# Kernel optimization log

Hardware: AMD Instinct MI355X
Metric: run time of the kernel (lower is better)

The kernel has to match this reference:

```python
import jax, jax.numpy as jnp
import numpy as np

BN_EPS = 1e-5


def conv2d(x, w, b, s, p):
    out = jax.lax.conv_general_dilated(
        x, w, (s, s), [(p, p), (p, p)],
        dimension_numbers=('NCHW', 'OIHW', 'NCHW'))
    return out + b[None, :, None, None]


def deform_conv2d(x, offset, mask, weight, s, p):
    # x: [B,C,H,W]; offset: [B,2*k*k,Ho,Wo] (y,x interleaved per tap);
    # mask: [B,k*k,Ho,Wo]; weight: [O,C,k,k]
    B, C, H, W = x.shape
    O, _, k, _ = weight.shape
    T = k * k
    Ho, Wo = offset.shape[2], offset.shape[3]
    off = offset.reshape(B, T, 2, Ho, Wo)
    ii = jnp.repeat(jnp.arange(k), k).astype(x.dtype)  # kernel row per tap
    jj = jnp.tile(jnp.arange(k), k).astype(x.dtype)    # kernel col per tap
    base_y = (jnp.arange(Ho) * s - p).astype(x.dtype)
    base_x = (jnp.arange(Wo) * s - p).astype(x.dtype)
    py = base_y[None, None, :, None] + ii[None, :, None, None] + off[:, :, 0]  # [B,T,Ho,Wo]
    px = base_x[None, None, None, :] + jj[None, :, None, None] + off[:, :, 1]
    y0 = jnp.floor(py)
    x0 = jnp.floor(px)
    ly = py - y0
    lx = px - x0
    y0i = y0.astype(jnp.int32)
    x0i = x0.astype(jnp.int32)
    x_flat = x.reshape(B, C, H * W)

    def gather(yy, xx):
        valid = ((yy >= 0) & (yy < H) & (xx >= 0) & (xx < W)).astype(x.dtype)
        idx = jnp.clip(yy, 0, H - 1) * W + jnp.clip(xx, 0, W - 1)
        idx_f = jnp.broadcast_to(idx.reshape(B, 1, -1), (B, C, T * Ho * Wo))
        g = jnp.take_along_axis(x_flat, idx_f, axis=2).reshape(B, C, T, Ho, Wo)
        return g * valid[:, None]

    val = (((1 - ly) * (1 - lx))[:, None] * gather(y0i, x0i)
           + ((1 - ly) * lx)[:, None] * gather(y0i, x0i + 1)
           + (ly * (1 - lx))[:, None] * gather(y0i + 1, x0i)
           + (ly * lx)[:, None] * gather(y0i + 1, x0i + 1))
    val = val * mask[:, None]  # modulated samples [B,C,T,Ho,Wo]
    w_flat = weight.reshape(O, C, T)
    return jnp.einsum('bcthw,oct->bohw', val, w_flat)


def setup_inputs() -> dict:
    key = jax.random.key(0)
    ks = jax.random.split(key, 8)
    B, C1, C2, H, W, k = 4, 128, 128, 64, 64, 3
    fan_in = C1 * k * k
    return {
        'x': jax.random.normal(ks[0], (B, C1, H, W), jnp.float32),
        'offset_w': 0.01 * jax.random.normal(ks[1], (2 * k * k, C1, k, k), jnp.float32),
        'offset_b': jnp.zeros((2 * k * k,), jnp.float32),
        'mask_w': 0.01 * jax.random.normal(ks[2], (k * k, C1, k, k), jnp.float32),
        'mask_b': jnp.zeros((k * k,), jnp.float32),
        'weight': jax.random.normal(ks[3], (C2, C1, k, k), jnp.float32) / np.sqrt(fan_in),
        'bn_gamma': 0.5 + jax.random.uniform(ks[4], (C2,), jnp.float32),
        'bn_beta': 0.1 * jax.random.normal(ks[5], (C2,), jnp.float32),
        'bn_mean': 0.1 * jax.random.normal(ks[6], (C2,), jnp.float32),
        'bn_var': 0.5 + jax.random.uniform(ks[7], (C2,), jnp.float32),
    }


def reference(x, offset_w, offset_b, mask_w, mask_b, weight,
              bn_gamma, bn_beta, bn_mean, bn_var):
    s, p = 1, 1
    offset = conv2d(x, offset_w, offset_b, s, p)
    mask = jax.nn.sigmoid(conv2d(x, mask_w, mask_b, s, p))
    out = deform_conv2d(x, offset, mask, weight, s, p)
    scale = bn_gamma / jnp.sqrt(bn_var + BN_EPS)
    out = (out - bn_mean[None, :, None, None]) * scale[None, :, None, None] \
        + bn_beta[None, :, None, None]
    return out * jax.nn.sigmoid(out)  # SiLU
```

## Files before the change

### kernel.cpp

```cpp
#include <hip/hip_runtime.h>
#include <math.h>

typedef unsigned short u16;
typedef short bf16x8 __attribute__((ext_vector_type(8)));
typedef float f32x4 __attribute__((ext_vector_type(4)));

#define XT_B   0u
#define WF_B   4194304u
#define WRF_B  4489216u
#define BNS_B  4562944u
#define BNB_B  4563456u

__device__ __forceinline__ u16 f2bf(float f) {
  union { float f; unsigned int i; } v; v.f = f;
  unsigned int i = v.i;
  return (u16)((i + 0x7fffu + ((i >> 16) & 1u)) >> 16);
}
__device__ __forceinline__ float ulo(unsigned int u) {
  union { unsigned int i; float f; } v; v.i = u << 16; return v.f;
}
__device__ __forceinline__ float uhi(unsigned int u) {
  union { unsigned int i; float f; } v; v.i = u & 0xffff0000u; return v.f;
}
__device__ __forceinline__ unsigned int pk(float lo, float hi) {
  return (unsigned int)f2bf(lo) | ((unsigned int)f2bf(hi) << 16);
}

__global__ __launch_bounds__(256) void prep_kernel(
    const float* __restrict__ x,   const float* __restrict__ ow,
    const float* __restrict__ mw,  const float* __restrict__ wgt,
    const float* __restrict__ gam, const float* __restrict__ bet,
    const float* __restrict__ mean,const float* __restrict__ var,
    char* __restrict__ wsb) {
  int blk = blockIdx.x, tid = threadIdx.x;
  if (blk < 512) {
    __shared__ u16 tile[32][136];
    int b = blk >> 7, y = (blk >> 1) & 63, xh = blk & 1;
    const float* src = x + (size_t)b * 524288 + y * 64 + xh * 32;
#pragma unroll
    for (int r = 0; r < 4; ++r) {
      int flat = r * 256 + tid;
      int c = flat >> 3, x4 = (flat & 7) * 4;
      float4 v = *(const float4*)(src + c * 4096 + x4);
      tile[x4 + 0][c] = f2bf(v.x);
      tile[x4 + 1][c] = f2bf(v.y);
      tile[x4 + 2][c] = f2bf(v.z);
      tile[x4 + 3][c] = f2bf(v.w);
    }
    __syncthreads();
    u16* dst = (u16*)(wsb + XT_B) + ((b * 64 + y) * 64 + xh * 32) * 128;
#pragma unroll
    for (int r = 0; r < 2; ++r) {
      int flat = r * 256 + tid;
      int xx = flat >> 4, c8 = (flat & 15) * 8;
      *(uint4*)(dst + xx * 128 + c8) = *(const uint4*)&tile[xx][c8];
    }
  } else if (blk < 1088) {
    int idx = (blk - 512) * 256 + tid;
    int jj = idx & 7, l = (idx >> 3) & 63, ks = (idx >> 9) & 3,
        mt = (idx >> 11) & 7, t = idx >> 14;
    int o = mt * 16 + (l & 15);
    int c = ks * 32 + (l >> 4) * 8 + jj;
    ((u16*)(wsb + WF_B))[idx] = f2bf(wgt[(o * 128 + c) * 9 + t]);
  } else if (blk < 1232) {
    int idx = (blk - 1088) * 256 + tid;
    int jj = idx & 7, l = (idx >> 3) & 63, mt = (idx >> 9) & 1, ks = idx >> 10;
    int oc = mt * 16 + (l & 15);
    int k = ks * 32 + (l >> 4) * 8 + jj;
    int t = k >> 7, c = k & 127;
    float v = 0.f;
    if (oc < 18) v = ow[(oc * 128 + c) * 9 + t];
    else if (oc < 27) v = mw[((oc - 18) * 128 + c) * 9 + t];
    ((u16*)(wsb + WRF_B))[idx] = f2bf(v);
  } else {
    if (tid < 128) {
      float s = gam[tid] * rsqrtf(var[tid] + 1e-5f);
      ((float*)(wsb + BNS_B))[tid] = s;
      ((float*)(wsb + BNB_B))[tid] = bet[tid] - mean[tid] * s;
    }
  }
}

__global__ __launch_bounds__(256, 4) void main_kernel(
    const char* __restrict__ wsb, const float* __restrict__ ob,
    const float* __restrict__ mb, float* __restrict__ out) {
  __shared__ __align__(16) char smem[16 * 1160 * 2];
  __shared__ float soff[16][32];
  u16* vbuf = (u16*)smem;
  float* pred = (float*)smem;

  int blk = blockIdx.x;
  int b = blk >> 8, ho = (blk >> 2) & 63, qd = blk & 3;
  int p0 = qd * 16;
  int tid = threadIdx.x;
  int w = tid >> 6, l = tid & 63, quad = l >> 4, pn = l & 15;

  const u16* XT = (const u16*)(wsb + XT_B);
  const bf16x8* WFv = (const bf16x8*)(wsb + WF_B);
  const bf16x8* WRFv = (const bf16x8*)(wsb + WRF_B);
  bf16x8 bz = {0, 0, 0, 0, 0, 0, 0, 0};

  {
    int mt = w & 1, kh = w >> 1;
    f32x4 acc = {0.f, 0.f, 0.f, 0.f};
#pragma unroll
    for (int t = 0; t < 9; ++t) {
      int y = ho + t / 3 - 1;
      int xx = p0 + pn + t % 3 - 1;
      bool valid = ((unsigned)y < 64u) && ((unsigned)xx < 64u);
      const u16* bp = XT + ((b * 64 + y) * 64 + xx) * 128 + quad * 8;
#pragma unroll
      for (int kqi = 0; kqi < 2; ++kqi) {
        int kq = kh * 2 + kqi;
        bf16x8 a = WRFv[((t * 4 + kq) * 2 + mt) * 64 + l];
        bf16x8 bb = valid ? *(const bf16x8*)(bp + kq * 32) : bz;
        acc = __builtin_amdgcn_mfma_f32_16x16x32_bf16(a, bb, acc, 0, 0, 0);
      }
    }
#pragma unroll
    for (int r = 0; r < 4; ++r)
      pred[((kh * 2 + mt) * 16 + quad * 4 + r) * 16 + pn] = acc[r];
  }
  __syncthreads();
  for (int i = tid; i < 432; i += 256) {
    int oc = i >> 4, p = i & 15;
    int mt = oc >> 4, row = oc & 15;
    float v = pred[(mt * 16 + row) * 16 + p] + pred[((2 + mt) * 16 + row) * 16 + p]
            + (oc < 18 ? ob[oc] : mb[oc - 18]);
    if (oc >= 18) v = 1.f / (1.f + __expf(-v));
    soff[p][oc] = v;
  }
  __syncthreads();

  {
    int cl = l & 15, pi = l >> 4;
    int p = w * 4 + pi;
    const u16* xb = XT + (size_t)b * 524288 + cl * 8;
#pragma unroll
    for (int t = 0; t < 9; ++t) {
      float oy = soff[p][2 * t], ox = soff[p][2 * t + 1], m = soff[p][18 + t];
      float py = (float)(ho + t / 3 - 1) + oy;
      float px = (float)(p0 + p + t % 3 - 1) + ox;
      float y0f = floorf(py), x0f = floorf(px);
      int y0 = (int)y0f, x0 = (int)x0f;
      float ly = py - y0f, lx = px - x0f;
      float vy0 = (y0 >= 0 && y0 < 64) ? 1.f : 0.f;
      float vy1 = (y0 >= -1 && y0 < 63) ? 1.f : 0.f;
      float vx0 = (x0 >= 0 && x0 < 64) ? 1.f : 0.f;
      float vx1 = (x0 >= -1 && x0 < 63) ? 1.f : 0.f;
      int y0c = min(max(y0, 0), 63), y1c = min(max(y0 + 1, 0), 63);
      int x0c = min(max(x0, 0), 63), x1c = min(max(x0 + 1, 0), 63);
      uint4 q00 = *(const uint4*)(xb + (y0c * 64 + x0c) * 128);
      uint4 q01 = *(const uint4*)(xb + (y0c * 64 + x1c) * 128);
      uint4 q10 = *(const uint4*)(xb + (y1c * 64 + x0c) * 128);
      uint4 q11 = *(const uint4*)(xb + (y1c * 64 + x1c) * 128);
      float w00 = (1.f - ly) * (1.f - lx) * m * vy0 * vx0;
      float w01 = (1.f - ly) * lx * m * vy0 * vx1;
      float w10 = ly * (1.f - lx) * m * vy1 * vx0;
      float w11 = ly * lx * m * vy1 * vx1;
      uint4 o;
      o.x = pk(w00 * ulo(q00.x) + w01 * ulo(q01.x) + w10 * ulo(q10.x) + w11 * ulo(q11.x),
               w00 * uhi(q00.x) + w01 * uhi(q01.x) + w10 * uhi(q10.x) + w11 * uhi(q11.x));
      o.y = pk(w00 * ulo(q00.y) + w01 * ulo(q01.y) + w10 * ulo(q10.y) + w11 * ulo(q11.y),
               w00 * uhi(q00.y) + w01 * uhi(q01.y) + w10 * uhi(q10.y) + w11 * uhi(q11.y));
      o.z = pk(w00 * ulo(q00.z) + w01 * ulo(q01.z) + w10 * ulo(q10.z) + w11 * ulo(q11.z),
               w00 * uhi(q00.z) + w01 * uhi(q01.z) + w10 * uhi(q10.z) + w11 * uhi(q11.z));
      o.w = pk(w00 * ulo(q00.w) + w01 * ulo(q01.w) + w10 * ulo(q10.w) + w11 * ulo(q11.w),
               w00 * uhi(q00.w) + w01 * uhi(q01.w) + w10 * uhi(q10.w) + w11 * uhi(q11.w));
      *(uint4*)&vbuf[p * 1160 + t * 128 + cl * 8] = o;
    }
  }
  __syncthreads();

  f32x4 acc0 = {0.f, 0.f, 0.f, 0.f}, acc1 = {0.f, 0.f, 0.f, 0.f};
  bf16x8 A0[2][4], A1[2][4];
#pragma unroll
  for (int ks = 0; ks < 4; ++ks) {
    A0[0][ks] = WFv[((0 * 8 + 2 * w) * 4 + ks) * 64 + l];
    A1[0][ks] = WFv[((0 * 8 + 2 * w + 1) * 4 + ks) * 64 + l];
  }
#pragma unroll
  for (int t = 0; t < 9; ++t) {
    int cur = t & 1, nxt = cur ^ 1;
    if (t < 8) {
#pragma unroll
      for (int ks = 0; ks < 4; ++ks) {
        A0[nxt][ks] = WFv[(((t + 1) * 8 + 2 * w) * 4 + ks) * 64 + l];
        A1[nxt][ks] = WFv[(((t + 1) * 8 + 2 * w + 1) * 4 + ks) * 64 + l];
      }
    }
#pragma unroll
    for (int ks = 0; ks < 4; ++ks) {
      bf16x8 bfr = *(const bf16x8*)&vbuf[pn * 1160 + t * 128 + ks * 32 + quad * 8];
      acc0 = __builtin_amdgcn_mfma_f32_16x16x32_bf16(A0[cur][ks], bfr, acc0, 0, 0, 0);
      acc1 = __builtin_amdgcn_mfma_f32_16x16x32_bf16(A1[cur][ks], bfr, acc1, 0, 0, 0);
    }
  }

  const float* BNS = (const float*)(wsb + BNS_B);
  const float* BNB = (const float*)(wsb + BNB_B);
#pragma unroll
  for (int mi = 0; mi < 2; ++mi) {
    f32x4 acc = mi ? acc1 : acc0;
#pragma unroll
    for (int r = 0; r < 4; ++r) {
      int o = (2 * w + mi) * 16 + quad * 4 + r;
      float v = acc[r] * BNS[o] + BNB[o];
      v = v / (1.f + __expf(-v));
      out[((b * 128 + o) * 64 + ho) * 64 + p0 + pn] = v;
    }
  }
}

extern "C" void kernel_launch(void* const* d_in, const int* in_sizes, int n_in,
                              void* d_out, int out_size, void* d_ws, size_t ws_size,
                              hipStream_t stream) {
  const float* x    = (const float*)d_in[0];
  const float* ow   = (const float*)d_in[1];
  const float* ob   = (const float*)d_in[2];
  const float* mw   = (const float*)d_in[3];
  const float* mb   = (const float*)d_in[4];
  const float* wgt  = (const float*)d_in[5];
  const float* gam  = (const float*)d_in[6];
  const float* bet  = (const float*)d_in[7];
  const float* mean = (const float*)d_in[8];
  const float* var  = (const float*)d_in[9];
  char* wsb = (char*)d_ws;
  float* out = (float*)d_out;

  prep_kernel<<<1233, 256, 0, stream>>>(x, ow, mw, wgt, gam, bet, mean, var, wsb);
  main_kernel<<<1024, 256, 0, stream>>>(wsb, ob, mb, out);
}
```

Measured before the change: 106.1 us.

## Double block tile to 32 pixels with 8 waves and software-pipeline bilinear gathers

Each block now covers 32 output pixels with 512 threads. Each wave owns one 16-channel output tile and reuses its weight fragments across two pixel tiles, which halves per-wave global weight loads. The bilinear-sampling loop is software-pipelined so the gathers for tap t+1 are issued before tap t is combined, hiding gather latency. The cost is twice the LDS per block, higher register pressure, and only 512 blocks, which lowers occupancy and grid parallelism.

```diff
diff --git a/kernel.cpp b/kernel.cpp
--- a/kernel.cpp
+++ b/kernel.cpp
@@ -81,17 +81,17 @@
   }
 }
 
-__global__ __launch_bounds__(256, 4) void main_kernel(
+__global__ __launch_bounds__(512, 4) void main_kernel(
     const char* __restrict__ wsb, const float* __restrict__ ob,
     const float* __restrict__ mb, float* __restrict__ out) {
-  __shared__ __align__(16) char smem[16 * 1160 * 2];
-  __shared__ float soff[16][32];
+  __shared__ __align__(16) char smem[32 * 1160 * 2];
+  __shared__ float soff[32][32];
   u16* vbuf = (u16*)smem;
   float* pred = (float*)smem;
 
   int blk = blockIdx.x;
-  int b = blk >> 8, ho = (blk >> 2) & 63, qd = blk & 3;
-  int p0 = qd * 16;
+  int b = blk >> 7, ho = (blk >> 1) & 63, half = blk & 1;
+  int p0 = half * 32;
   int tid = threadIdx.x;
   int w = tid >> 6, l = tid & 63, quad = l >> 4, pn = l & 15;
 
@@ -101,12 +101,13 @@
   bf16x8 bz = {0, 0, 0, 0, 0, 0, 0, 0};
 
   {
-    int mt = w & 1, kh = w >> 1;
+    int mt = w & 1, nt = (w >> 1) & 1, kh = w >> 2;
+    int p = nt * 16 + pn;
     f32x4 acc = {0.f, 0.f, 0.f, 0.f};
 #pragma unroll
     for (int t = 0; t < 9; ++t) {
       int y = ho + t / 3 - 1;
-      int xx = p0 + pn + t % 3 - 1;
+      int xx = p0 + p + t % 3 - 1;
       bool valid = ((unsigned)y < 64u) && ((unsigned)xx < 64u);
       const u16* bp = XT + ((b * 64 + y) * 64 + xx) * 128 + quad * 8;
 #pragma unroll
@@ -119,13 +120,14 @@
     }
 #pragma unroll
     for (int r = 0; r < 4; ++r)
-      pred[((kh * 2 + mt) * 16 + quad * 4 + r) * 16 + pn] = acc[r];
+      pred[(((kh * 2 + mt) * 2 + nt) * 16 + quad * 4 + r) * 16 + pn] = acc[r];
   }
   __syncthreads();
-  for (int i = tid; i < 432; i += 256) {
-    int oc = i >> 4, p = i & 15;
-    int mt = oc >> 4, row = oc & 15;
-    float v = pred[(mt * 16 + row) * 16 + p] + pred[((2 + mt) * 16 + row) * 16 + p]
+  for (int i = tid; i < 864; i += 512) {
+    int oc = i >> 5, p = i & 31;
+    int mt = oc >> 4, row = oc & 15, nt = p >> 4, pn2 = p & 15;
+    float v = pred[((mt * 2 + nt) * 16 + row) * 16 + pn2]
+            + pred[(((2 + mt) * 2 + nt) * 16 + row) * 16 + pn2]
             + (oc < 18 ? ob[oc] : mb[oc - 18]);
     if (oc >= 18) v = 1.f / (1.f + __expf(-v));
     soff[p][oc] = v;
@@ -136,8 +138,10 @@
     int cl = l & 15, pi = l >> 4;
     int p = w * 4 + pi;
     const u16* xb = XT + (size_t)b * 524288 + cl * 8;
-#pragma unroll
-    for (int t = 0; t < 9; ++t) {
+    uint4 q00[2], q01[2], q10[2], q11[2];
+    float w00[2], w01[2], w10[2], w11[2];
+
+    auto issue = [&](int t, int st) {
       float oy = soff[p][2 * t], ox = soff[p][2 * t + 1], m = soff[p][18 + t];
       float py = (float)(ho + t / 3 - 1) + oy;
       float px = (float)(p0 + p + t % 3 - 1) + ox;
@@ -150,64 +154,70 @@
       float vx1 = (x0 >= -1 && x0 < 63) ? 1.f : 0.f;
       int y0c = min(max(y0, 0), 63), y1c = min(max(y0 + 1, 0), 63);
       int x0c = min(max(x0, 0), 63), x1c = min(max(x0 + 1, 0), 63);
-      uint4 q00 = *(const uint4*)(xb + (y0c * 64 + x0c) * 128);
-      uint4 q01 = *(const uint4*)(xb + (y0c * 64 + x1c) * 128);
-      uint4 q10 = *(const uint4*)(xb + (y1c * 64 + x0c) * 128);
-      uint4 q11 = *(const uint4*)(xb + (y1c * 64 + x1c) * 128);
-      float w00 = (1.f - ly) * (1.f - lx) * m * vy0 * vx0;
-      float w01 = (1.f - ly) * lx * m * vy0 * vx1;
-      float w10 = ly * (1.f - lx) * m * vy1 * vx0;
-      float w11 = ly * lx * m * vy1 * vx1;
+      q00[st] = *(const uint4*)(xb + (y0c * 64 + x0c) * 128);
+      q01[st] = *(const uint4*)(xb + (y0c * 64 + x1c) * 128);
+      q10[st] = *(const uint4*)(xb + (y1c * 64 + x0c) * 128);
+      q11[st] = *(const uint4*)(xb + (y1c * 64 + x1c) * 128);
+      w00[st] = (1.f - ly) * (1.f - lx) * m * vy0 * vx0;
+      w01[st] = (1.f - ly) * lx * m * vy0 * vx1;
+      w10[st] = ly * (1.f - lx) * m * vy1 * vx0;
+      w11[st] = ly * lx * m * vy1 * vx1;
+    };
+
+    issue(0, 0);
+#pragma unroll
+    for (int t = 0; t < 9; ++t) {
+      int cur = t & 1;
+      if (t < 8) issue(t + 1, cur ^ 1);
+      float a00 = w00[cur], a01 = w01[cur], a10 = w10[cur], a11 = w11[cur];
+      uint4 c00 = q00[cur], c01 = q01[cur], c10 = q10[cur], c11 = q11[cur];
       uint4 o;
-      o.x = pk(w00 * ulo(q00.x) + w01 * ulo(q01.x) + w10 * ulo(q10.x) + w11 * ulo(q11.x),
-               w00 * uhi(q00.x) + w01 * uhi(q01.x) + w10 * uhi(q10.x) + w11 * uhi(q11.x));
-      o.y = pk(w00 * ulo(q00.y) + w01 * ulo(q01.y) + w10 * ulo(q10.y) + w11 * ulo(q11.y),
-               w00 * uhi(q00.y) + w01 * uhi(q01.y) + w10 * uhi(q10.y) + w11 * uhi(q11.y));
-      o.z = pk(w00 * ulo(q00.z) + w01 * ulo(q01.z) + w10 * ulo(q10.z) + w11 * ulo(q11.z),
-               w00 * uhi(q00.z) + w01 * uhi(q01.z) + w10 * uhi(q10.z) + w11 * uhi(q11.z));
-      o.w = pk(w00 * ulo(q00.w) + w01 * ulo(q01.w) + w10 * ulo(q10.w) + w11 * ulo(q11.w),
-               w00 * uhi(q00.w) + w01 * uhi(q01.w) + w10 * uhi(q10.w) + w11 * uhi(q11.w));
+      o.x = pk(a00 * ulo(c00.x) + a01 * ulo(c01.x) + a10 * ulo(c10.x) + a11 * ulo(c11.x),
+               a00 * uhi(c00.x) + a01 * uhi(c01.x) + a10 * uhi(c10.x) + a11 * uhi(c11.x));
+      o.y = pk(a00 * ulo(c00.y) + a01 * ulo(c01.y) + a10 * ulo(c10.y) + a11 * ulo(c11.y),
+               a00 * uhi(c00.y) + a01 * uhi(c01.y) + a10 * uhi(c10.y) + a11 * uhi(c11.y));
+      o.z = pk(a00 * ulo(c00.z) + a01 * ulo(c01.z) + a10 * ulo(c10.z) + a11 * ulo(c11.z),
+               a00 * uhi(c00.z) + a01 * uhi(c01.z) + a10 * uhi(c10.z) + a11 * uhi(c11.z));
+      o.w = pk(a00 * ulo(c00.w) + a01 * ulo(c01.w) + a10 * ulo(c10.w) + a11 * ulo(c11.w),
+               a00 * uhi(c00.w) + a01 * uhi(c01.w) + a10 * uhi(c10.w) + a11 * uhi(c11.w));
       *(uint4*)&vbuf[p * 1160 + t * 128 + cl * 8] = o;
     }
   }
   __syncthreads();
 
   f32x4 acc0 = {0.f, 0.f, 0.f, 0.f}, acc1 = {0.f, 0.f, 0.f, 0.f};
-  bf16x8 A0[2][4], A1[2][4];
-#pragma unroll
-  for (int ks = 0; ks < 4; ++ks) {
-    A0[0][ks] = WFv[((0 * 8 + 2 * w) * 4 + ks) * 64 + l];
-    A1[0][ks] = WFv[((0 * 8 + 2 * w + 1) * 4 + ks) * 64 + l];
-  }
+  bf16x8 A[2][4];
+#pragma unroll
+  for (int ks = 0; ks < 4; ++ks)
+    A[0][ks] = WFv[((0 * 8 + w) * 4 + ks) * 64 + l];
 #pragma unroll
   for (int t = 0; t < 9; ++t) {
     int cur = t & 1, nxt = cur ^ 1;
     if (t < 8) {
 #pragma unroll
-      for (int ks = 0; ks < 4; ++ks) {
-        A0[nxt][ks] = WFv[(((t + 1) * 8 + 2 * w) * 4 + ks) * 64 + l];
-        A1[nxt][ks] = WFv[(((t + 1) * 8 + 2 * w + 1) * 4 + ks) * 64 + l];
-      }
+      for (int ks = 0; ks < 4; ++ks)
+        A[nxt][ks] = WFv[(((t + 1) * 8 + w) * 4 + ks) * 64 + l];
     }
 #pragma unroll
     for (int ks = 0; ks < 4; ++ks) {
-      bf16x8 bfr = *(const bf16x8*)&vbuf[pn * 1160 + t * 128 + ks * 32 + quad * 8];
-      acc0 = __builtin_amdgcn_mfma_f32_16x16x32_bf16(A0[cur][ks], bfr, acc0, 0, 0, 0);
-      acc1 = __builtin_amdgcn_mfma_f32_16x16x32_bf16(A1[cur][ks], bfr, acc1, 0, 0, 0);
+      bf16x8 b0 = *(const bf16x8*)&vbuf[pn * 1160 + t * 128 + ks * 32 + quad * 8];
+      bf16x8 b1 = *(const bf16x8*)&vbuf[(16 + pn) * 1160 + t * 128 + ks * 32 + quad * 8];
+      acc0 = __builtin_amdgcn_mfma_f32_16x16x32_bf16(A[cur][ks], b0, acc0, 0, 0, 0);
+      acc1 = __builtin_amdgcn_mfma_f32_16x16x32_bf16(A[cur][ks], b1, acc1, 0, 0, 0);
     }
   }
 
   const float* BNS = (const float*)(wsb + BNS_B);
   const float* BNB = (const float*)(wsb + BNB_B);
 #pragma unroll
-  for (int mi = 0; mi < 2; ++mi) {
-    f32x4 acc = mi ? acc1 : acc0;
+  for (int nt = 0; nt < 2; ++nt) {
+    f32x4 acc = nt ? acc1 : acc0;
 #pragma unroll
     for (int r = 0; r < 4; ++r) {
-      int o = (2 * w + mi) * 16 + quad * 4 + r;
+      int o = w * 16 + quad * 4 + r;
       float v = acc[r] * BNS[o] + BNB[o];
       v = v / (1.f + __expf(-v));
-      out[((b * 128 + o) * 64 + ho) * 64 + p0 + pn] = v;
+      out[((b * 128 + o) * 64 + ho) * 64 + p0 + nt * 16 + pn] = v;
     }
   }
 }
@@ -229,5 +239,5 @@
   float* out = (float*)d_out;
 
   prep_kernel<<<1233, 256, 0, stream>>>(x, ow, mw, wgt, gam, bet, mean, var, wsb);
-  main_kernel<<<1024, 256, 0, stream>>>(wsb, ob, mb, out);
-}
+  main_kernel<<<512, 512, 0, stream>>>(wsb, ob, mb, out);
+}
```

Measured after the change: 105.6 us. No clear change (-0.5%).

## Feed bilinear samples directly into MFMA with split-K across waves

Applied to the files above, without the earlier changes.

The main kernel no longer stages the modulated bilinear samples in a shared-memory buffer. Each wave now owns a 32-channel slice of K and feeds the freshly computed bf16 fragment straight into MFMAs for all 8 output tiles, holding 8 accumulators per wave. The partial sums from the four waves are reduced through a padded shared array before BN and SiLU. This removes the LDS write/read round trip and one barrier, at the cost of more accumulator registers (and possible occupancy loss) plus a cross-wave reduction. Weight fragments are now loaded inline per tap instead of being double-buffered.

```diff
diff --git a/kernel.cpp b/kernel.cpp
--- a/kernel.cpp
+++ b/kernel.cpp
@@ -84,10 +84,9 @@
 __global__ __launch_bounds__(256, 4) void main_kernel(
     const char* __restrict__ wsb, const float* __restrict__ ob,
     const float* __restrict__ mb, float* __restrict__ out) {
-  __shared__ __align__(16) char smem[16 * 1160 * 2];
-  __shared__ float soff[16][32];
-  u16* vbuf = (u16*)smem;
-  float* pred = (float*)smem;
+  __shared__ __align__(16) float red[4][8][16][17];
+  __shared__ float sofft[28 * 17];
+  float* pred = &red[0][0][0][0];
 
   int blk = blockIdx.x;
   int b = blk >> 8, ho = (blk >> 2) & 63, qd = blk & 3;
@@ -128,19 +127,22 @@
     float v = pred[(mt * 16 + row) * 16 + p] + pred[((2 + mt) * 16 + row) * 16 + p]
             + (oc < 18 ? ob[oc] : mb[oc - 18]);
     if (oc >= 18) v = 1.f / (1.f + __expf(-v));
-    soff[p][oc] = v;
+    sofft[oc * 17 + p] = v;
   }
   __syncthreads();
 
+  f32x4 acc[8];
+#pragma unroll
+  for (int ot = 0; ot < 8; ++ot) acc[ot] = (f32x4){0.f, 0.f, 0.f, 0.f};
   {
-    int cl = l & 15, pi = l >> 4;
-    int p = w * 4 + pi;
-    const u16* xb = XT + (size_t)b * 524288 + cl * 8;
+    const u16* xb = XT + (size_t)b * 524288 + w * 32 + quad * 8;
 #pragma unroll
     for (int t = 0; t < 9; ++t) {
-      float oy = soff[p][2 * t], ox = soff[p][2 * t + 1], m = soff[p][18 + t];
+      float oy = sofft[(2 * t) * 17 + pn];
+      float ox = sofft[(2 * t + 1) * 17 + pn];
+      float m  = sofft[(18 + t) * 17 + pn];
       float py = (float)(ho + t / 3 - 1) + oy;
-      float px = (float)(p0 + p + t % 3 - 1) + ox;
+      float px = (float)(p0 + pn + t % 3 - 1) + ox;
       float y0f = floorf(py), x0f = floorf(px);
       int y0 = (int)y0f, x0 = (int)x0f;
       float ly = py - y0f, lx = px - x0f;
@@ -158,57 +160,42 @@
       float w01 = (1.f - ly) * lx * m * vy0 * vx1;
       float w10 = ly * (1.f - lx) * m * vy1 * vx0;
       float w11 = ly * lx * m * vy1 * vx1;
-      uint4 o;
-      o.x = pk(w00 * ulo(q00.x) + w01 * ulo(q01.x) + w10 * ulo(q10.x) + w11 * ulo(q11.x),
-               w00 * uhi(q00.x) + w01 * uhi(q01.x) + w10 * uhi(q10.x) + w11 * uhi(q11.x));
-      o.y = pk(w00 * ulo(q00.y) + w01 * ulo(q01.y) + w10 * ulo(q10.y) + w11 * ulo(q11.y),
-               w00 * uhi(q00.y) + w01 * uhi(q01.y) + w10 * uhi(q10.y) + w11 * uhi(q11.y));
-      o.z = pk(w00 * ulo(q00.z) + w01 * ulo(q01.z) + w10 * ulo(q10.z) + w11 * ulo(q11.z),
-               w00 * uhi(q00.z) + w01 * uhi(q01.z) + w10 * uhi(q10.z) + w11 * uhi(q11.z));
-      o.w = pk(w00 * ulo(q00.w) + w01 * ulo(q01.w) + w10 * ulo(q10.w) + w11 * ulo(q11.w),
-               w00 * uhi(q00.w) + w01 * uhi(q01.w) + w10 * uhi(q10.w) + w11 * uhi(q11.w));
-      *(uint4*)&vbuf[p * 1160 + t * 128 + cl * 8] = o;
-    }
-  }
+      union { uint4 u; bf16x8 v; } bq;
+      bq.u.x = pk(w00 * ulo(q00.x) + w01 * ulo(q01.x) + w10 * ulo(q10.x) + w11 * ulo(q11.x),
+                  w00 * uhi(q00.x) + w01 * uhi(q01.x) + w10 * uhi(q10.x) + w11 * uhi(q11.x));
+      bq.u.y = pk(w00 * ulo(q00.y) + w01 * ulo(q01.y) + w10 * ulo(q10.y) + w11 * ulo(q11.y),
+                  w00 * uhi(q00.y) + w01 * uhi(q01.y) + w10 * uhi(q10.y) + w11 * uhi(q11.y));
+      bq.u.z = pk(w00 * ulo(q00.z) + w01 * ulo(q01.z) + w10 * ulo(q10.z) + w11 * ulo(q11.z),
+                  w00 * uhi(q00.z) + w01 * uhi(q01.z) + w10 * uhi(q10.z) + w11 * uhi(q11.z));
+      bq.u.w = pk(w00 * ulo(q00.w) + w01 * ulo(q01.w) + w10 * ulo(q10.w) + w11 * ulo(q11.w),
+                  w00 * uhi(q00.w) + w01 * uhi(q01.w) + w10 * uhi(q10.w) + w11 * uhi(q11.w));
+#pragma unroll
+      for (int ot = 0; ot < 8; ++ot) {
+        bf16x8 a = WFv[((t * 8 + ot) * 4 + w) * 64 + l];
+        acc[ot] = __builtin_amdgcn_mfma_f32_16x16x32_bf16(a, bq.v, acc[ot], 0, 0, 0);
+      }
+    }
+  }
+
+#pragma unroll
+  for (int ot = 0; ot < 8; ++ot)
+#pragma unroll
+    for (int r = 0; r < 4; ++r)
+      red[w][ot][quad * 4 + r][pn] = acc[ot][r];
   __syncthreads();
-
-  f32x4 acc0 = {0.f, 0.f, 0.f, 0.f}, acc1 = {0.f, 0.f, 0.f, 0.f};
-  bf16x8 A0[2][4], A1[2][4];
-#pragma unroll
-  for (int ks = 0; ks < 4; ++ks) {
-    A0[0][ks] = WFv[((0 * 8 + 2 * w) * 4 + ks) * 64 + l];
-    A1[0][ks] = WFv[((0 * 8 + 2 * w + 1) * 4 + ks) * 64 + l];
-  }
-#pragma unroll
-  for (int t = 0; t < 9; ++t) {
-    int cur = t & 1, nxt = cur ^ 1;
-    if (t < 8) {
-#pragma unroll
-      for (int ks = 0; ks < 4; ++ks) {
-        A0[nxt][ks] = WFv[(((t + 1) * 8 + 2 * w) * 4 + ks) * 64 + l];
-        A1[nxt][ks] = WFv[(((t + 1) * 8 + 2 * w + 1) * 4 + ks) * 64 + l];
-      }
-    }
-#pragma unroll
-    for (int ks = 0; ks < 4; ++ks) {
-      bf16x8 bfr = *(const bf16x8*)&vbuf[pn * 1160 + t * 128 + ks * 32 + quad * 8];
-      acc0 = __builtin_amdgcn_mfma_f32_16x16x32_bf16(A0[cur][ks], bfr, acc0, 0, 0, 0);
-      acc1 = __builtin_amdgcn_mfma_f32_16x16x32_bf16(A1[cur][ks], bfr, acc1, 0, 0, 0);
-    }
-  }
 
   const float* BNS = (const float*)(wsb + BNS_B);
   const float* BNB = (const float*)(wsb + BNB_B);
 #pragma unroll
-  for (int mi = 0; mi < 2; ++mi) {
-    f32x4 acc = mi ? acc1 : acc0;
-#pragma unroll
-    for (int r = 0; r < 4; ++r) {
-      int o = (2 * w + mi) * 16 + quad * 4 + r;
-      float v = acc[r] * BNS[o] + BNB[o];
-      v = v / (1.f + __expf(-v));
-      out[((b * 128 + o) * 64 + ho) * 64 + p0 + pn] = v;
-    }
+  for (int i = 0; i < 8; ++i) {
+    int idx = i * 256 + tid;
+    int o = idx >> 4, p = idx & 15;
+    int ot = o >> 4, row = o & 15;
+    float s = red[0][ot][row][p] + red[1][ot][row][p]
+            + red[2][ot][row][p] + red[3][ot][row][p];
+    float v = s * BNS[o] + BNB[o];
+    v = v / (1.f + __expf(-v));
+    out[((b * 128 + o) * 64 + ho) * 64 + p0 + p] = v;
   }
 }
 
```

New measurement: 116.2 us. +9.5%, slower.

## Double threads per block and split offset conv, sampling and GEMM across 8 waves

Applied to the files above, without the earlier changes.

Raises the main kernel from 256 to 512 threads (8 waves) with the same 16-pixel tile. The offset/mask conv now splits K four ways across waves and reduces 4 partials. The bilinear sampling splits the 9 taps between two wave halves, and the output GEMM gives each wave one 16-channel tile instead of two. The offset buffer is transposed with padding to avoid bank conflicts. The aim is more waves in flight to hide gather latency and fewer registers per thread. The costs are more block-level sync overhead, a higher occupancy target in the launch bounds that may force register limits, and less ILP per wave.

```diff
diff --git a/kernel.cpp b/kernel.cpp
--- a/kernel.cpp
+++ b/kernel.cpp
@@ -81,13 +81,12 @@
   }
 }
 
-__global__ __launch_bounds__(256, 4) void main_kernel(
+__global__ __launch_bounds__(512, 8) void main_kernel(
     const char* __restrict__ wsb, const float* __restrict__ ob,
     const float* __restrict__ mb, float* __restrict__ out) {
-  __shared__ __align__(16) char smem[16 * 1160 * 2];
-  __shared__ float soff[16][32];
-  u16* vbuf = (u16*)smem;
-  float* pred = (float*)smem;
+  __shared__ __align__(16) u16 vbuf[16 * 1160];
+  __shared__ float sofft[28 * 17];
+  float* pred = (float*)vbuf;
 
   int blk = blockIdx.x;
   int b = blk >> 8, ho = (blk >> 2) & 63, qd = blk & 3;
@@ -101,7 +100,7 @@
   bf16x8 bz = {0, 0, 0, 0, 0, 0, 0, 0};
 
   {
-    int mt = w & 1, kh = w >> 1;
+    int mt = w & 1, kq = w >> 1;
     f32x4 acc = {0.f, 0.f, 0.f, 0.f};
 #pragma unroll
     for (int t = 0; t < 9; ++t) {
@@ -109,36 +108,41 @@
       int xx = p0 + pn + t % 3 - 1;
       bool valid = ((unsigned)y < 64u) && ((unsigned)xx < 64u);
       const u16* bp = XT + ((b * 64 + y) * 64 + xx) * 128 + quad * 8;
-#pragma unroll
-      for (int kqi = 0; kqi < 2; ++kqi) {
-        int kq = kh * 2 + kqi;
-        bf16x8 a = WRFv[((t * 4 + kq) * 2 + mt) * 64 + l];
-        bf16x8 bb = valid ? *(const bf16x8*)(bp + kq * 32) : bz;
-        acc = __builtin_amdgcn_mfma_f32_16x16x32_bf16(a, bb, acc, 0, 0, 0);
-      }
+      bf16x8 a = WRFv[((t * 4 + kq) * 2 + mt) * 64 + l];
+      bf16x8 bb = valid ? *(const bf16x8*)(bp + kq * 32) : bz;
+      acc = __builtin_amdgcn_mfma_f32_16x16x32_bf16(a, bb, acc, 0, 0, 0);
     }
 #pragma unroll
     for (int r = 0; r < 4; ++r)
-      pred[((kh * 2 + mt) * 16 + quad * 4 + r) * 16 + pn] = acc[r];
+      pred[(w * 16 + quad * 4 + r) * 16 + pn] = acc[r];
   }
   __syncthreads();
-  for (int i = tid; i < 432; i += 256) {
-    int oc = i >> 4, p = i & 15;
+  if (tid < 432) {
+    int oc = tid >> 4, p = tid & 15;
     int mt = oc >> 4, row = oc & 15;
-    float v = pred[(mt * 16 + row) * 16 + p] + pred[((2 + mt) * 16 + row) * 16 + p]
+    float v = pred[((0 * 2 + mt) * 16 + row) * 16 + p]
+            + pred[((1 * 2 + mt) * 16 + row) * 16 + p]
+            + pred[((2 * 2 + mt) * 16 + row) * 16 + p]
+            + pred[((3 * 2 + mt) * 16 + row) * 16 + p]
             + (oc < 18 ? ob[oc] : mb[oc - 18]);
     if (oc >= 18) v = 1.f / (1.f + __expf(-v));
-    soff[p][oc] = v;
+    sofft[oc * 17 + p] = v;
   }
   __syncthreads();
 
   {
+    int th = w >> 2, wl = w & 3;
     int cl = l & 15, pi = l >> 4;
-    int p = w * 4 + pi;
+    int p = wl * 4 + pi;
     const u16* xb = XT + (size_t)b * 524288 + cl * 8;
-#pragma unroll
-    for (int t = 0; t < 9; ++t) {
-      float oy = soff[p][2 * t], ox = soff[p][2 * t + 1], m = soff[p][18 + t];
+    int ntap = th ? 4 : 5;
+#pragma unroll
+    for (int i = 0; i < 5; ++i) {
+      if (i >= ntap) break;
+      int t = th + 2 * i;
+      float oy = sofft[(2 * t) * 17 + p];
+      float ox = sofft[(2 * t + 1) * 17 + p];
+      float m  = sofft[(18 + t) * 17 + p];
       float py = (float)(ho + t / 3 - 1) + oy;
       float px = (float)(p0 + p + t % 3 - 1) + ox;
       float y0f = floorf(py), x0f = floorf(px);
@@ -172,43 +176,34 @@
   }
   __syncthreads();
 
-  f32x4 acc0 = {0.f, 0.f, 0.f, 0.f}, acc1 = {0.f, 0.f, 0.f, 0.f};
-  bf16x8 A0[2][4], A1[2][4];
-#pragma unroll
-  for (int ks = 0; ks < 4; ++ks) {
-    A0[0][ks] = WFv[((0 * 8 + 2 * w) * 4 + ks) * 64 + l];
-    A1[0][ks] = WFv[((0 * 8 + 2 * w + 1) * 4 + ks) * 64 + l];
-  }
+  f32x4 acc = {0.f, 0.f, 0.f, 0.f};
+  bf16x8 A[2][4];
+#pragma unroll
+  for (int ks = 0; ks < 4; ++ks)
+    A[0][ks] = WFv[((0 * 8 + w) * 4 + ks) * 64 + l];
 #pragma unroll
   for (int t = 0; t < 9; ++t) {
     int cur = t & 1, nxt = cur ^ 1;
     if (t < 8) {
 #pragma unroll
-      for (int ks = 0; ks < 4; ++ks) {
-        A0[nxt][ks] = WFv[(((t + 1) * 8 + 2 * w) * 4 + ks) * 64 + l];
-        A1[nxt][ks] = WFv[(((t + 1) * 8 + 2 * w + 1) * 4 + ks) * 64 + l];
-      }
+      for (int ks = 0; ks < 4; ++ks)
+        A[nxt][ks] = WFv[(((t + 1) * 8 + w) * 4 + ks) * 64 + l];
     }
 #pragma unroll
     for (int ks = 0; ks < 4; ++ks) {
       bf16x8 bfr = *(const bf16x8*)&vbuf[pn * 1160 + t * 128 + ks * 32 + quad * 8];
-      acc0 = __builtin_amdgcn_mfma_f32_16x16x32_bf16(A0[cur][ks], bfr, acc0, 0, 0, 0);
-      acc1 = __builtin_amdgcn_mfma_f32_16x16x32_bf16(A1[cur][ks], bfr, acc1, 0, 0, 0);
+      acc = __builtin_amdgcn_mfma_f32_16x16x32_bf16(A[cur][ks], bfr, acc, 0, 0, 0);
     }
   }
 
   const float* BNS = (const float*)(wsb + BNS_B);
   const float* BNB = (const float*)(wsb + BNB_B);
 #pragma unroll
-  for (int mi = 0; mi < 2; ++mi) {
-    f32x4 acc = mi ? acc1 : acc0;
-#pragma unroll
-    for (int r = 0; r < 4; ++r) {
-      int o = (2 * w + mi) * 16 + quad * 4 + r;
-      float v = acc[r] * BNS[o] + BNB[o];
-      v = v / (1.f + __expf(-v));
-      out[((b * 128 + o) * 64 + ho) * 64 + p0 + pn] = v;
-    }
+  for (int r = 0; r < 4; ++r) {
+    int o = w * 16 + quad * 4 + r;
+    float v = acc[r] * BNS[o] + BNB[o];
+    v = v / (1.f + __expf(-v));
+    out[((b * 128 + o) * 64 + ho) * 64 + p0 + pn] = v;
   }
 }
 
@@ -229,5 +224,5 @@
   float* out = (float*)d_out;
 
   prep_kernel<<<1233, 256, 0, stream>>>(x, ow, mw, wgt, gam, bet, mean, var, wsb);
-  main_kernel<<<1024, 256, 0, stream>>>(wsb, ob, mb, out);
-}
+  main_kernel<<<1024, 512, 0, stream>>>(wsb, ob, mb, out);
+}
```

Result: slower. 109.7 us (+3.4%).
